# Kernel tuning notes

Measured on AMD Instinct MI355X. Metric: run time of the kernel, lower is better.

The kernel has to match this reference:

```python
import jax, jax.numpy as jnp
import numpy as np


def setup_inputs() -> dict:
    key = jax.random.key(0)
    k1, k2 = jax.random.split(key)
    N, D, E = 8192, 4096, 16
    x = jax.random.normal(k1, (N, D), dtype=jnp.float32)
    Wg = jax.random.normal(k2, (E, D), dtype=jnp.float32) * (1.0 / np.sqrt(D))
    return {"x": x, "Wg": Wg, "k": 2}


def reference(x, Wg, k):
    # Router logits and gates (fp32, matching input.float() + Linear.float())
    logits = jnp.einsum("nd,ed->ne", x.astype(jnp.float32), Wg)  # [N, E]
    gates = jax.nn.softmax(logits, axis=1)
    N, E = gates.shape

    # top-k expert selection; concat column-wise like torch chunk(k, dim=1)
    _, topk_idx = jax.lax.top_k(gates, k)            # [N, k]
    idx = topk_idx.T.reshape(-1)                     # [k*N] token->expert

    # one-hot masks for each of the k choices, concatenated along token dim
    mask = jax.nn.one_hot(idx, E, dtype=jnp.int32)   # [k*N, E]

    # gate weights for each choice; normalize across the k=2 choices
    w_cols = jnp.take_along_axis(gates, topk_idx, axis=1)  # [N, k]
    w_norm = w_cols[:, 0] + w_cols[:, 1]
    weight = (w_cols / w_norm[:, None]).T.reshape(-1)      # [k*N]

    # expert token counts and within-expert positions (cumsum trick)
    expert_token_count = jnp.sum(mask, axis=0)                       # [E]
    pos_in_expert = jnp.sum((jnp.cumsum(mask, axis=0) - 1) * mask, axis=1)  # [k*N]

    # load-balancing aux loss uses only the top-1 mask
    me = jnp.mean(gates, axis=0)
    ce = jnp.mean(mask[:N].astype(jnp.float32), axis=0)
    l_aux = jnp.sum(me * ce) * E

    # exclusive cumsum of expert counts -> base offset per expert
    expert_offset = jnp.cumsum(expert_token_count) - expert_token_count
    token_pos_after = pos_in_expert + expert_offset[idx]             # [k*N]

    token_num = N * k
    token_pos_before = jnp.zeros((token_num,), dtype=jnp.int32).at[token_pos_after].set(
        jnp.arange(token_num, dtype=jnp.int32)
    )
    return (l_aux, token_pos_after, token_pos_before, expert_token_count, weight)
```

## Files before the change

kernel.cpp:

```cpp
#include <hip/hip_runtime.h>
#include <math.h>

#define N_TOK 8192
#define DIM   4096
#define NE    16
#define TOKS  (2*N_TOK)
#define NCHUNK (TOKS/64)
#define D4    (DIM/4)
#define NSEGG 8
#define SLICEF4 128

#define OUT_LAUX 0
#define OUT_TPA  1
#define OUT_TPB  (1+TOKS)
#define OUT_CNT  (1+2*TOKS)
#define OUT_W    (1+2*TOKS+NE)

__global__ __launch_bounds__(256) void k1_rowlane(
    const float4* __restrict__ x4, const float4* __restrict__ wg4,
    float* __restrict__ part)
{
    __shared__ float4 wgl[NE][SLICEF4];
    __shared__ float  pl[4][64][NE];

    const int tid  = threadIdx.x;
    const int lane = tid & 63;
    const int w    = tid >> 6;
    const int g    = blockIdx.x & 7;
    const int rg   = blockIdx.x >> 3;

    #pragma unroll
    for (int i = 0; i < 8; ++i) {
        const int idx = i * 256 + tid;
        const int e = idx >> 7, c = idx & 127;
        wgl[e][c] = wg4[(size_t)e * D4 + g * SLICEF4 + c];
    }
    __syncthreads();

    const int row = rg * 64 + lane;
    const float4* xrow = x4 + (size_t)row * D4 + g * SLICEF4 + w * 32;

    float acc[NE];
    #pragma unroll
    for (int e = 0; e < NE; ++e) acc[e] = 0.f;

    #pragma unroll
    for (int si = 0; si < 4; ++si) {
        float4 xq[8];
        #pragma unroll
        for (int k = 0; k < 8; ++k) xq[k] = xrow[si * 8 + k];
        #pragma unroll
        for (int e = 0; e < NE; ++e) {
            float a = acc[e];
            #pragma unroll
            for (int k = 0; k < 8; ++k) {
                const float4 wv = wgl[e][w * 32 + si * 8 + k];
                a = fmaf(xq[k].x, wv.x, a);
                a = fmaf(xq[k].y, wv.y, a);
                a = fmaf(xq[k].z, wv.z, a);
                a = fmaf(xq[k].w, wv.w, a);
            }
            acc[e] = a;
        }
    }

    #pragma unroll
    for (int e = 0; e < NE; ++e) pl[w][lane][e] = acc[e];
    __syncthreads();

    #pragma unroll
    for (int j = 0; j < 4; ++j) {
        const int flat = j * 256 + tid;
        const int r = flat >> 4, e = flat & 15;
        const float s = pl[0][r][e] + pl[1][r][e] + pl[2][r][e] + pl[3][r][e];
        part[(size_t)g * (N_TOK * NE) + (size_t)rg * 1024 + flat] = s;
    }
}

__global__ __launch_bounds__(128) void k2_route(
    const float* __restrict__ part, int* __restrict__ pr,
    int* __restrict__ hist, float* __restrict__ me_part,
    float* __restrict__ out)
{
    const int row   = blockIdx.x * 128 + threadIdx.x;
    const int lane  = threadIdx.x & 63;
    const int gwave = row >> 6;

    float lg[NE];
    #pragma unroll
    for (int e = 0; e < NE; ++e) lg[e] = 0.f;
    const float4* p4 = (const float4*)part;
    #pragma unroll
    for (int s = 0; s < NSEGG; ++s) {
        const size_t base = ((size_t)s * N_TOK + row) * 4;
        #pragma unroll
        for (int q = 0; q < 4; ++q) {
            float4 t = p4[base + q];
            lg[q * 4 + 0] += t.x;
            lg[q * 4 + 1] += t.y;
            lg[q * 4 + 2] += t.z;
            lg[q * 4 + 3] += t.w;
        }
    }

    float m1 = -INFINITY; int i1 = 0;
    #pragma unroll
    for (int e = 0; e < NE; ++e)
        if (lg[e] > m1) { m1 = lg[e]; i1 = e; }
    float m2 = -INFINITY; int i2 = 0;
    #pragma unroll
    for (int e = 0; e < NE; ++e)
        if (e != i1 && lg[e] > m2) { m2 = lg[e]; i2 = e; }

    float ssum = 0.f, ex[NE];
    #pragma unroll
    for (int e = 0; e < NE; ++e) { ex[e] = __expf(lg[e] - m1); ssum += ex[e]; }
    const float inv = 1.f / ssum;

    const float e2v = __expf(m2 - m1);
    const float w1  = 1.f / (1.f + e2v);
    out[OUT_W + row]         = w1;
    out[OUT_W + N_TOK + row] = 1.f - w1;

    float mymev = 0.f;
    #pragma unroll
    for (int e = 0; e < NE; ++e) {
        float mv = ex[e] * inv;
        mv += __shfl_xor(mv, 32); mv += __shfl_xor(mv, 16);
        mv += __shfl_xor(mv, 8);  mv += __shfl_xor(mv, 4);
        mv += __shfl_xor(mv, 2);  mv += __shfl_xor(mv, 1);
        if (lane == e) mymev = mv;
    }
    if (lane < NE) me_part[gwave * NE + lane] = mymev;

    const unsigned long long mlt = (1ull << lane) - 1ull;
    int rk1 = 0, rk2 = 0;
    #pragma unroll
    for (int eo = 0; eo < NE; ++eo) {
        unsigned long long mA = __ballot(i1 == eo);
        unsigned long long mB = __ballot(i2 == eo);
        if (i1 == eo) rk1 = (int)__popcll(mA & mlt);
        if (i2 == eo) rk2 = (int)__popcll(mB & mlt);
        if (lane == eo) {
            hist[gwave * NE + eo]                = (int)__popcll(mA);
            hist[(NCHUNK / 2 + gwave) * NE + eo] = (int)__popcll(mB);
        }
    }
    pr[row]         = i1 | (rk1 << 8);
    pr[N_TOK + row] = i2 | (rk2 << 8);
}

__global__ __launch_bounds__(256) void k3_place(
    const int* __restrict__ pr, const int* __restrict__ hist,
    const float* __restrict__ me_part, float* __restrict__ out)
{
    __shared__ int   sh[NCHUNK][20];
    __shared__ int   cnt_sh[NE], ce_sh[NE];
    __shared__ float me_sh[16][17];
    __shared__ float me_tot[NE];

    const int t = threadIdx.x;

    int h[NE];
    {
        const int4* h4 = (const int4*)(hist + t * NE);
        int4 a = h4[0], b = h4[1], c = h4[2], d = h4[3];
        h[0]=a.x; h[1]=a.y; h[2]=a.z; h[3]=a.w;
        h[4]=b.x; h[5]=b.y; h[6]=b.z; h[7]=b.w;
        h[8]=c.x; h[9]=c.y; h[10]=c.z; h[11]=c.w;
        h[12]=d.x; h[13]=d.y; h[14]=d.z; h[15]=d.w;
    }
    #pragma unroll
    for (int e = 0; e < NE; ++e) sh[t][e] = h[e];
    __syncthreads();

    for (int off = 1; off < NCHUNK; off <<= 1) {
        int tmp[NE];
        #pragma unroll
        for (int e = 0; e < NE; ++e) tmp[e] = (t >= off) ? sh[t - off][e] : 0;
        __syncthreads();
        #pragma unroll
        for (int e = 0; e < NE; ++e) sh[t][e] += tmp[e];
        __syncthreads();
    }

    if (t == NCHUNK - 1) {
        #pragma unroll
        for (int e = 0; e < NE; ++e) cnt_sh[e] = sh[t][e];
    }
    if (t == NCHUNK / 2 - 1) {
        #pragma unroll
        for (int e = 0; e < NE; ++e) ce_sh[e] = sh[t][e];
    }

    int ex[NE];
    #pragma unroll
    for (int e = 0; e < NE; ++e) ex[e] = sh[t][e] - h[e];
    __syncthreads();
    #pragma unroll
    for (int e = 0; e < NE; ++e) sh[t][e] = ex[e];
    __syncthreads();

    int offs[NE];
    {
        int run = 0;
        #pragma unroll
        for (int e = 0; e < NE; ++e) { offs[e] = run; run += cnt_sh[e]; }
    }

    {
        const int tk = blockIdx.x * 256 + t;
        const int v  = pr[tk];
        const int e  = v & 255;
        const int rk = v >> 8;
        const int c  = tk >> 6;
        const int pos = sh[c][e] + offs[e] + rk;
        out[OUT_TPA + tk]  = (float)pos;
        out[OUT_TPB + pos] = (float)tk;
    }

    if (blockIdx.x == 0) {
        {
            const int e = t & 15, gg = t >> 4;
            float s = 0.f;
            #pragma unroll
            for (int k = 0; k < 8; ++k) s += me_part[(gg + 16 * k) * NE + e];
            me_sh[gg][e] = s;
        }
        __syncthreads();
        if (t < NE) {
            float me = 0.f;
            #pragma unroll
            for (int gg = 0; gg < 16; ++gg) me += me_sh[gg][t];
            me_tot[t] = me;
            out[OUT_CNT + t] = (float)cnt_sh[t];
        }
        __syncthreads();
        if (t == 0) {
            float la = 0.f;
            #pragma unroll
            for (int e = 0; e < NE; ++e)
                la += (me_tot[e] * (1.0f / N_TOK)) * ((float)ce_sh[e] * (1.0f / N_TOK));
            out[OUT_LAUX] = la * (float)NE;
        }
    }
}

extern "C" void kernel_launch(void* const* d_in, const int* in_sizes, int n_in,
                              void* d_out, int out_size, void* d_ws, size_t ws_size,
                              hipStream_t stream) {
    const float* x  = (const float*)d_in[0];
    const float* wg = (const float*)d_in[1];
    float* out = (float*)d_out;

    char* w = (char*)d_ws;
    float* part    = (float*)w;  w += (size_t)NSEGG * N_TOK * NE * sizeof(float);
    int*   pr      = (int*)w;    w += TOKS * sizeof(int);
    int*   hist    = (int*)w;    w += NCHUNK * NE * sizeof(int);
    float* me_part = (float*)w;

    k1_rowlane<<<(N_TOK / 64) * NSEGG, 256, 0, stream>>>(
        (const float4*)x, (const float4*)wg, part);
    k2_route<<<N_TOK / 128, 128, 0, stream>>>(part, pr, hist, me_part, out);
    k3_place<<<TOKS / 256, 256, 0, stream>>>(pr, hist, me_part, out);
}
```

Baseline: 214.0 us.

## Process two row groups per block to reuse LDS gate weights

The router GEMV kernel now computes 128 rows per block instead of 64, so each lane accumulates two rows against the same LDS-resident weight slice. This halves the number of blocks that reload the weight slice and reuses each LDS read for twice the FMAs. The weight buffer and the partial-sum buffer now share LDS through a union, and the partial buffer is transposed and padded. The route kernel switches to 64-thread blocks. Costs are doubled accumulator and x registers, which may lower occupancy, and half as many k1 blocks to fill the GPU.

```diff
diff --git a/kernel.cpp b/kernel.cpp
--- a/kernel.cpp
+++ b/kernel.cpp
@@ -9,6 +9,7 @@
 #define D4    (DIM/4)
 #define NSEGG 8
 #define SLICEF4 128
+#define RPB   128
 
 #define OUT_LAUX 0
 #define OUT_TPA  1
@@ -20,8 +21,10 @@
     const float4* __restrict__ x4, const float4* __restrict__ wg4,
     float* __restrict__ part)
 {
-    __shared__ float4 wgl[NE][SLICEF4];
-    __shared__ float  pl[4][64][NE];
+    __shared__ union {
+        float4 wgl[NE][SLICEF4];
+        float  pl[4][NE][RPB + 1];
+    } sm;
 
     const int tid  = threadIdx.x;
     const int lane = tid & 63;
@@ -33,56 +36,69 @@
     for (int i = 0; i < 8; ++i) {
         const int idx = i * 256 + tid;
         const int e = idx >> 7, c = idx & 127;
-        wgl[e][c] = wg4[(size_t)e * D4 + g * SLICEF4 + c];
-    }
-    __syncthreads();
-
-    const int row = rg * 64 + lane;
-    const float4* xrow = x4 + (size_t)row * D4 + g * SLICEF4 + w * 32;
-
-    float acc[NE];
-    #pragma unroll
-    for (int e = 0; e < NE; ++e) acc[e] = 0.f;
+        sm.wgl[e][c] = wg4[(size_t)e * D4 + g * SLICEF4 + c];
+    }
+    __syncthreads();
+
+    const int row0 = rg * RPB + lane;
+    const float4* xrowA = x4 + (size_t)row0 * D4 + g * SLICEF4 + w * 32;
+    const float4* xrowB = xrowA + (size_t)64 * D4;
+
+    float accA[NE], accB[NE];
+    #pragma unroll
+    for (int e = 0; e < NE; ++e) { accA[e] = 0.f; accB[e] = 0.f; }
 
     #pragma unroll
     for (int si = 0; si < 4; ++si) {
-        float4 xq[8];
-        #pragma unroll
-        for (int k = 0; k < 8; ++k) xq[k] = xrow[si * 8 + k];
+        float4 xa[8], xb[8];
+        #pragma unroll
+        for (int k = 0; k < 8; ++k) {
+            xa[k] = xrowA[si * 8 + k];
+            xb[k] = xrowB[si * 8 + k];
+        }
         #pragma unroll
         for (int e = 0; e < NE; ++e) {
-            float a = acc[e];
+            float a = accA[e], b = accB[e];
             #pragma unroll
             for (int k = 0; k < 8; ++k) {
-                const float4 wv = wgl[e][w * 32 + si * 8 + k];
-                a = fmaf(xq[k].x, wv.x, a);
-                a = fmaf(xq[k].y, wv.y, a);
-                a = fmaf(xq[k].z, wv.z, a);
-                a = fmaf(xq[k].w, wv.w, a);
+                const float4 wv = sm.wgl[e][w * 32 + si * 8 + k];
+                a = fmaf(xa[k].x, wv.x, a);
+                a = fmaf(xa[k].y, wv.y, a);
+                a = fmaf(xa[k].z, wv.z, a);
+                a = fmaf(xa[k].w, wv.w, a);
+                b = fmaf(xb[k].x, wv.x, b);
+                b = fmaf(xb[k].y, wv.y, b);
+                b = fmaf(xb[k].z, wv.z, b);
+                b = fmaf(xb[k].w, wv.w, b);
             }
-            acc[e] = a;
-        }
-    }
-
-    #pragma unroll
-    for (int e = 0; e < NE; ++e) pl[w][lane][e] = acc[e];
-    __syncthreads();
-
-    #pragma unroll
-    for (int j = 0; j < 4; ++j) {
+            accA[e] = a; accB[e] = b;
+        }
+    }
+
+    __syncthreads();
+    #pragma unroll
+    for (int e = 0; e < NE; ++e) {
+        sm.pl[w][e][lane]      = accA[e];
+        sm.pl[w][e][64 + lane] = accB[e];
+    }
+    __syncthreads();
+
+    #pragma unroll
+    for (int j = 0; j < 8; ++j) {
         const int flat = j * 256 + tid;
         const int r = flat >> 4, e = flat & 15;
-        const float s = pl[0][r][e] + pl[1][r][e] + pl[2][r][e] + pl[3][r][e];
-        part[(size_t)g * (N_TOK * NE) + (size_t)rg * 1024 + flat] = s;
-    }
-}
-
-__global__ __launch_bounds__(128) void k2_route(
+        const float s = sm.pl[0][e][r] + sm.pl[1][e][r]
+                      + sm.pl[2][e][r] + sm.pl[3][e][r];
+        part[(size_t)g * (N_TOK * NE) + (size_t)rg * (RPB * NE) + flat] = s;
+    }
+}
+
+__global__ __launch_bounds__(64) void k2_route(
     const float* __restrict__ part, int* __restrict__ pr,
     int* __restrict__ hist, float* __restrict__ me_part,
     float* __restrict__ out)
 {
-    const int row   = blockIdx.x * 128 + threadIdx.x;
+    const int row   = blockIdx.x * 64 + threadIdx.x;
     const int lane  = threadIdx.x & 63;
     const int gwave = row >> 6;
 
@@ -259,8 +275,8 @@
     int*   hist    = (int*)w;    w += NCHUNK * NE * sizeof(int);
     float* me_part = (float*)w;
 
-    k1_rowlane<<<(N_TOK / 64) * NSEGG, 256, 0, stream>>>(
+    k1_rowlane<<<(N_TOK / RPB) * NSEGG, 256, 0, stream>>>(
         (const float4*)x, (const float4*)wg, part);
-    k2_route<<<N_TOK / 128, 128, 0, stream>>>(part, pr, hist, me_part, out);
+    k2_route<<<N_TOK / 64, 64, 0, stream>>>(part, pr, hist, me_part, out);
     k3_place<<<TOKS / 256, 256, 0, stream>>>(pr, hist, me_part, out);
 }
```

Result: no change. 217.3 us (+1.6%).

## Regroup GEMV lanes as 4 threads per row with shuffle reduction

Applied to the files above, without the earlier changes.

Remaps the k1 work so that each wave handles 16 rows, with 4 lanes per row reading interleaved float4 columns. Neighbouring lanes now read contiguous 64-byte runs of x instead of rows that sit 16 KB apart. The shared-memory cross-wave reduction and its sync are replaced by two xor shuffles plus a float4 store per lane. The trade-off is that LDS reads of Wg now differ across lanes (4 distinct addresses per wave instead of a broadcast), which may add LDS traffic or bank conflicts.

```diff
diff --git a/kernel.cpp b/kernel.cpp
--- a/kernel.cpp
+++ b/kernel.cpp
@@ -16,29 +16,30 @@
 #define OUT_CNT  (1+2*TOKS)
 #define OUT_W    (1+2*TOKS+NE)
 
-__global__ __launch_bounds__(256) void k1_rowlane(
+__global__ __launch_bounds__(256) void k1_grouped(
     const float4* __restrict__ x4, const float4* __restrict__ wg4,
     float* __restrict__ part)
 {
     __shared__ float4 wgl[NE][SLICEF4];
-    __shared__ float  pl[4][64][NE];
 
     const int tid  = threadIdx.x;
     const int lane = tid & 63;
     const int w    = tid >> 6;
+    const int r    = lane >> 2;
+    const int c    = lane & 3;
     const int g    = blockIdx.x & 7;
     const int rg   = blockIdx.x >> 3;
 
     #pragma unroll
     for (int i = 0; i < 8; ++i) {
         const int idx = i * 256 + tid;
-        const int e = idx >> 7, c = idx & 127;
-        wgl[e][c] = wg4[(size_t)e * D4 + g * SLICEF4 + c];
-    }
-    __syncthreads();
-
-    const int row = rg * 64 + lane;
-    const float4* xrow = x4 + (size_t)row * D4 + g * SLICEF4 + w * 32;
+        const int e = idx >> 7, cc = idx & 127;
+        wgl[e][cc] = wg4[(size_t)e * D4 + g * SLICEF4 + cc];
+    }
+    __syncthreads();
+
+    const int row = rg * 64 + w * 16 + r;
+    const float4* xrow = x4 + (size_t)row * D4 + g * SLICEF4 + c;
 
     float acc[NE];
     #pragma unroll
@@ -48,13 +49,13 @@
     for (int si = 0; si < 4; ++si) {
         float4 xq[8];
         #pragma unroll
-        for (int k = 0; k < 8; ++k) xq[k] = xrow[si * 8 + k];
+        for (int k = 0; k < 8; ++k) xq[k] = xrow[4 * (si * 8 + k)];
         #pragma unroll
         for (int e = 0; e < NE; ++e) {
             float a = acc[e];
             #pragma unroll
             for (int k = 0; k < 8; ++k) {
-                const float4 wv = wgl[e][w * 32 + si * 8 + k];
+                const float4 wv = wgl[e][c + 4 * (si * 8 + k)];
                 a = fmaf(xq[k].x, wv.x, a);
                 a = fmaf(xq[k].y, wv.y, a);
                 a = fmaf(xq[k].z, wv.z, a);
@@ -64,17 +65,21 @@
         }
     }
 
-    #pragma unroll
-    for (int e = 0; e < NE; ++e) pl[w][lane][e] = acc[e];
-    __syncthreads();
-
-    #pragma unroll
-    for (int j = 0; j < 4; ++j) {
-        const int flat = j * 256 + tid;
-        const int r = flat >> 4, e = flat & 15;
-        const float s = pl[0][r][e] + pl[1][r][e] + pl[2][r][e] + pl[3][r][e];
-        part[(size_t)g * (N_TOK * NE) + (size_t)rg * 1024 + flat] = s;
-    }
+    float red[NE];
+    #pragma unroll
+    for (int e = 0; e < NE; ++e) {
+        float v = acc[e];
+        v += __shfl_xor(v, 1);
+        v += __shfl_xor(v, 2);
+        red[e] = v;
+    }
+
+    float4 o;
+    o.x = (c == 0) ? red[0] : (c == 1) ? red[4] : (c == 2) ? red[8]  : red[12];
+    o.y = (c == 0) ? red[1] : (c == 1) ? red[5] : (c == 2) ? red[9]  : red[13];
+    o.z = (c == 0) ? red[2] : (c == 1) ? red[6] : (c == 2) ? red[10] : red[14];
+    o.w = (c == 0) ? red[3] : (c == 1) ? red[7] : (c == 2) ? red[11] : red[15];
+    ((float4*)part)[(size_t)g * (N_TOK * 4) + (size_t)row * 4 + c] = o;
 }
 
 __global__ __launch_bounds__(128) void k2_route(
@@ -259,7 +264,7 @@
     int*   hist    = (int*)w;    w += NCHUNK * NE * sizeof(int);
     float* me_part = (float*)w;
 
-    k1_rowlane<<<(N_TOK / 64) * NSEGG, 256, 0, stream>>>(
+    k1_grouped<<<(N_TOK / 64) * NSEGG, 256, 0, stream>>>(
         (const float4*)x, (const float4*)wg, part);
     k2_route<<<N_TOK / 128, 128, 0, stream>>>(part, pr, hist, me_part, out);
     k3_place<<<TOKS / 256, 256, 0, stream>>>(pr, hist, me_part, out);
```

Result: no change. 210.1 us (median of 2 runs) (-1.8%).

## Coalesce x loads in router GEMV with 16-lane shuffle reduction per row

Applied to the files above, without the earlier changes.

The first kernel now assigns 16 lanes to each row, so a wavefront reads contiguous float4 chunks of x instead of 64 rows at one stride each. Partial dot products are reduced with xor shuffles, which removes the shared-memory cross-wave reduction and its barrier. This costs extra shuffle work per expert and keeps 16 lanes busy per output. The routing kernel also moves to 64-thread blocks, which doubles its block count.

```diff
diff --git a/kernel.cpp b/kernel.cpp
--- a/kernel.cpp
+++ b/kernel.cpp
@@ -16,73 +16,67 @@
 #define OUT_CNT  (1+2*TOKS)
 #define OUT_W    (1+2*TOKS+NE)
 
-__global__ __launch_bounds__(256) void k1_rowlane(
+__global__ __launch_bounds__(256) void k1_coal(
     const float4* __restrict__ x4, const float4* __restrict__ wg4,
     float* __restrict__ part)
 {
     __shared__ float4 wgl[NE][SLICEF4];
-    __shared__ float  pl[4][64][NE];
 
     const int tid  = threadIdx.x;
     const int lane = tid & 63;
     const int w    = tid >> 6;
+    const int r    = lane >> 4;
+    const int c    = lane & 15;
     const int g    = blockIdx.x & 7;
     const int rg   = blockIdx.x >> 3;
 
     #pragma unroll
     for (int i = 0; i < 8; ++i) {
         const int idx = i * 256 + tid;
-        const int e = idx >> 7, c = idx & 127;
-        wgl[e][c] = wg4[(size_t)e * D4 + g * SLICEF4 + c];
-    }
-    __syncthreads();
-
-    const int row = rg * 64 + lane;
-    const float4* xrow = x4 + (size_t)row * D4 + g * SLICEF4 + w * 32;
-
-    float acc[NE];
-    #pragma unroll
-    for (int e = 0; e < NE; ++e) acc[e] = 0.f;
-
-    #pragma unroll
-    for (int si = 0; si < 4; ++si) {
+        const int e = idx >> 7, cc = idx & 127;
+        wgl[e][cc] = wg4[(size_t)e * D4 + g * SLICEF4 + cc];
+    }
+    __syncthreads();
+
+    const int rowbase = rg * 64 + w * 16;
+
+    #pragma unroll
+    for (int j = 0; j < 4; ++j) {
+        const int row = rowbase + j * 4 + r;
+        const float4* xrow = x4 + (size_t)row * D4 + g * SLICEF4 + c;
+
         float4 xq[8];
         #pragma unroll
-        for (int k = 0; k < 8; ++k) xq[k] = xrow[si * 8 + k];
+        for (int k = 0; k < 8; ++k) xq[k] = xrow[16 * k];
+
+        float red = 0.f;
         #pragma unroll
         for (int e = 0; e < NE; ++e) {
-            float a = acc[e];
+            float a = 0.f;
             #pragma unroll
             for (int k = 0; k < 8; ++k) {
-                const float4 wv = wgl[e][w * 32 + si * 8 + k];
+                const float4 wv = wgl[e][c + 16 * k];
                 a = fmaf(xq[k].x, wv.x, a);
                 a = fmaf(xq[k].y, wv.y, a);
                 a = fmaf(xq[k].z, wv.z, a);
                 a = fmaf(xq[k].w, wv.w, a);
             }
-            acc[e] = a;
-        }
-    }
-
-    #pragma unroll
-    for (int e = 0; e < NE; ++e) pl[w][lane][e] = acc[e];
-    __syncthreads();
-
-    #pragma unroll
-    for (int j = 0; j < 4; ++j) {
-        const int flat = j * 256 + tid;
-        const int r = flat >> 4, e = flat & 15;
-        const float s = pl[0][r][e] + pl[1][r][e] + pl[2][r][e] + pl[3][r][e];
-        part[(size_t)g * (N_TOK * NE) + (size_t)rg * 1024 + flat] = s;
-    }
-}
-
-__global__ __launch_bounds__(128) void k2_route(
+            a += __shfl_xor(a, 1);
+            a += __shfl_xor(a, 2);
+            a += __shfl_xor(a, 4);
+            a += __shfl_xor(a, 8);
+            if (c == e) red = a;
+        }
+        part[(size_t)g * (N_TOK * NE) + (size_t)row * NE + c] = red;
+    }
+}
+
+__global__ __launch_bounds__(64) void k2_route(
     const float* __restrict__ part, int* __restrict__ pr,
     int* __restrict__ hist, float* __restrict__ me_part,
     float* __restrict__ out)
 {
-    const int row   = blockIdx.x * 128 + threadIdx.x;
+    const int row   = blockIdx.x * 64 + threadIdx.x;
     const int lane  = threadIdx.x & 63;
     const int gwave = row >> 6;
 
@@ -259,8 +253,8 @@
     int*   hist    = (int*)w;    w += NCHUNK * NE * sizeof(int);
     float* me_part = (float*)w;
 
-    k1_rowlane<<<(N_TOK / 64) * NSEGG, 256, 0, stream>>>(
+    k1_coal<<<(N_TOK / 64) * NSEGG, 256, 0, stream>>>(
         (const float4*)x, (const float4*)wg, part);
-    k2_route<<<N_TOK / 128, 128, 0, stream>>>(part, pr, hist, me_part, out);
+    k2_route<<<N_TOK / 64, 64, 0, stream>>>(part, pr, hist, me_part, out);
     k3_place<<<TOKS / 256, 256, 0, stream>>>(pr, hist, me_part, out);
 }
```

Result: slower. 683.3 us (+219.3%).
